# Optimization experiments

Hardware: AMD Instinct MI355X
Metric: run time of the kernel (lower is better)

The kernel has to match this reference:

```python
import jax, jax.numpy as jnp
import numpy as np

LARGENUMBER = 10000.0
B, L = 32, 128


def setup_inputs() -> dict:
    key = jax.random.key(0)
    k1, k2 = jax.random.split(key)
    scores = jax.random.normal(k1, (B, L, L, 1), dtype=jnp.float32)
    seq_lens = jax.random.randint(k2, (B,), L // 2, L + 1).astype(jnp.int32)
    seq_lens = seq_lens.at[0].set(L)  # module assumes max(seq_lens) == matrix dim
    return {"span_mention_score_matrix": scores, "sequence_lengths": seq_lens}


def _inside_logZ(scores, seq_lens):
    """CKY inside algorithm in the log semiring (the `coolio` path).

    Recurrence (combined mention/non-mention channels):
      A[i,i]  = log(1 + e^{s_ii})
      A[i,j]  = logsumexp_{k=i..j-1}(A[i,k] + A[k+1,j]) + log(1 + e^{s_ij})
      Z[b]    = A[b, 0, len_b - 1]
    """
    s = scores[..., 0]                      # (B, L, L)
    Bn, Ln = s.shape[0], s.shape[1]
    log1p_exp = jnp.log1p(jnp.exp(s))       # log(1 + e^s), multiplicative factor per span
    # init: logsumexp([score, 0 above/on diag | -LARGE below diag]) as in coolio
    tri = jnp.where(jnp.arange(Ln)[:, None] <= jnp.arange(Ln)[None, :], 0.0, -LARGENUMBER)
    A0 = jnp.logaddexp(s, tri[None])        # diagonal entries = log(1+e^s); upper entries get overwritten

    i_idx = jnp.arange(Ln)[:, None]         # (L, 1)   span start
    m_idx = jnp.arange(Ln - 1)[None, :]     # (1, L-1) split offset
    rows = jnp.arange(Ln)

    def body(A, w):
        # left child  A[i, i+m], right child A[i+m+1, i+w], m = 0..w-1
        jl = jnp.clip(i_idx + m_idx, 0, Ln - 1)
        ir = jnp.clip(i_idx + m_idx + 1, 0, Ln - 1)
        jr = jnp.clip(i_idx + w, 0, Ln - 1)
        left = A[:, i_idx, jl]              # (B, L, L-1)
        right = A[:, ir, jr]                # (B, L, L-1)
        mask = (m_idx < w) & (i_idx + w < Ln)
        vals = jnp.where(mask, left + right, -LARGENUMBER)
        S = jax.nn.logsumexp(vals, axis=2)  # (B, L) logbmm along diagonal w
        cols = jnp.clip(rows + w, 0, N := Ln - 1) if False else jnp.clip(rows + w, 0, Ln - 1)
        new = S + log1p_exp[:, rows, cols]
        valid = (rows + w) < Ln
        A = A.at[:, rows, cols].set(jnp.where(valid[None, :], new, A[:, rows, cols]))
        return A, None

    A, _ = jax.lax.scan(body, A0, jnp.arange(1, Ln))
    Z = A[jnp.arange(Bn), 0, seq_lens - 1]  # (B,)
    return Z


def reference(span_mention_score_matrix, sequence_lengths):
    # forward returns (log-partition Z, marginals = dZ.sum()/dscores), like coolio()
    Z, vjp_fn = jax.vjp(lambda sc: _inside_logZ(sc, sequence_lengths), span_mention_score_matrix)
    marginal = vjp_fn(jnp.ones_like(Z))[0][..., 0]  # (B, L, L)
    return Z, marginal
```

## Files before the change

### kernel.cpp

```cpp
#include <hip/hip_runtime.h>

#define LL  128
#define STR 131
#define NT  1024

__device__ __forceinline__ float softplus_f(float x) { return log1pf(__expf(x)); }

__device__ __forceinline__ void lds_barrier() {
    asm volatile("s_waitcnt lgkmcnt(0)" ::: "memory");
    __builtin_amdgcn_s_barrier();
    asm volatile("" ::: "memory");
}

extern "C" __global__ __launch_bounds__(NT, 1) void cky_kernel(
    const float* __restrict__ scores,
    const int* __restrict__ seq_lens,
    float* __restrict__ Z_out,
    float* __restrict__ marg_out)
{
    extern __shared__ float smem[];
    float* ALs = smem;
    float* SBs = smem + LL * STR;

    const int b   = blockIdx.x;
    const int tid = threadIdx.x;
    const int i   = tid >> 3;
    const int vl  = tid & 7;
    const float* s = scores + (size_t)b * LL * LL;
    float* marg = marg_out + (size_t)b * LL * LL;
    const int len = seq_lens[b];

    for (int idx = tid; idx < LL * LL; idx += NT) {
        const int r = idx >> 7, c = idx & 127;
        const float sp = softplus_f(s[idx]);
        if (c > r)       SBs[c * STR + r] = sp;
        else if (c == r) ALs[r * STR + r] = sp;
    }
    lds_barrier();

    const float Ai = ALs[i * STR + i];

    float bulk = 0.f, Mreg = Ai;
    if (i + 1 < len) {
        const int j = i + 1;
        const float S = Ai + ALs[j * STR + j];
        const float A = S + SBs[j * STR + i];
        if (vl == 0) {
            ALs[i * STR + j] = A;
            ALs[j * STR + i] = A;
            SBs[i * STR + j] = S;
        }
    }
    lds_barrier();

    for (int w = 2; w < len; ++w) {
        const int j = i + w;
        float a_jm1 = 0.f;
        if (j < len) {
            a_jm1 = ALs[i * STR + (j - 1)];
            const float a_ip1j = ALs[j * STR + (i + 1)];
            const float a_jj   = ALs[j * STR + j];
            const float spv    = SBs[j * STR + i];
            const float acc = bulk
                            + __expf(Ai    + a_ip1j - Mreg)
                            + __expf(a_jm1 + a_jj   - Mreg);
            const float S = Mreg + __logf(acc);
            const float A = S + spv;
            if (vl == 0) {
                ALs[i * STR + j] = A;
                ALs[j * STR + i] = A;
                SBs[i * STR + j] = S;
            }
        }
        float nb = 0.f;
        if (j + 1 < len) {
            const float M = a_jm1;
            const float* Arow = ALs + i * STR;
            const float* Amir = ALs + (j + 1) * STR;
            for (int k = i + 1 + vl; k <= j - 1; k += 8)
                nb += __expf(Arow[k] + Amir[k + 1] - M);
        }
        nb += __shfl_xor(nb, 1); nb += __shfl_xor(nb, 2); nb += __shfl_xor(nb, 4);
        bulk = nb; Mreg = a_jm1;
        lds_barrier();
    }

    if (tid == 0) Z_out[b] = ALs[len - 1];

    const float Arm1 = (i >= 1) ? ALs[(i - 1) * STR + (i - 1)] : 0.f;
    float gbulk = 0.f;
    for (int w = len - 2; w >= 0; --w) {
        const int c = i + w;
        if (c < len) {
            const float Aown  = ALs[i * STR + c];
            const float S_own = (w == 0) ? 0.f : SBs[i * STR + c];
            float acc = gbulk;
            if (c + 1 < len) {
                const float slL  = SBs[i * STR + (c + 1)];
                const float a_c1 = ALs[(c + 1) * STR + (c + 1)];
                acc += __expf(Aown + a_c1 - slL);
            }
            if (i >= 1) {
                const float slR = SBs[(i - 1) * STR + c];
                acc += __expf(Arm1 + Aown - slR);
            }
            const float SL = S_own - __logf(acc);
            if (vl == 0) SBs[i * STR + c] = SL;
        }
        float nb = 0.f;
        if (w >= 1) {
            const int c2 = i + w - 1;
            if (c2 < len) {
                const float Ao2 = ALs[i * STR + c2];
                const float* ArowC = ALs + (c2 + 1) * STR;
                const float* SLrow = SBs + i * STR;
                for (int J = c2 + 2 + vl; J < len; J += 8)
                    nb += __expf(Ao2 + ArowC[J] - SLrow[J]);
                if (i >= 2) {
                    const float* Amir = ALs + (i - 1) * STR;
                    for (int I = vl; I <= i - 2; I += 8)
                        nb += __expf(Amir[I] + Ao2 - SBs[I * STR + c2]);
                }
            }
        }
        nb += __shfl_xor(nb, 1); nb += __shfl_xor(nb, 2); nb += __shfl_xor(nb, 4);
        gbulk = nb;
        lds_barrier();
    }

    for (int idx = tid; idx < LL * LL; idx += NT) {
        const int r = idx >> 7, c = idx & 127;
        float m = 0.f;
        if (c >= r && c < len) {
            const float sp = softplus_f(s[idx]);
            const float G  = __expf(ALs[r * STR + c] - sp - SBs[r * STR + c]);
            m = G * (1.f - __expf(-sp));
        }
        marg[idx] = m;
    }
}

extern "C" void kernel_launch(void* const* d_in, const int* in_sizes, int n_in,
                              void* d_out, int out_size, void* d_ws, size_t ws_size,
                              hipStream_t stream) {
    const float* scores  = (const float*)d_in[0];
    const int* seq_lens  = (const int*)d_in[1];
    const int B = in_sizes[1];
    float* out = (float*)d_out;
    float* Z_out = out;
    float* marg  = out + B;

    const size_t lds_bytes = (size_t)2 * LL * STR * sizeof(float);
    hipFuncSetAttribute((const void*)cky_kernel,
                        hipFuncAttributeMaxDynamicSharedMemorySize,
                        (int)lds_bytes);
    cky_kernel<<<B, NT, lds_bytes, stream>>>(scores, seq_lens, Z_out, marg);
}
```

Baseline: 266.6 us.

## Adapt threads-per-cell group size per diagonal in CKY inside/outside passes

Replaces the fixed 8-lanes-per-span-start mapping with a per-diagonal group size chosen from the number of active cells, so short diagonals get up to 64 lanes each for the split reduction. Partial sums are carried across iterations through a small LDS array instead of registers, since the cell-to-thread mapping now changes each step. This targets idle threads and long serial inner loops on the later diagonals, which dominate the sequential wavefront. In exchange it adds per-iteration group-size computation, wider shuffle reductions and an extra LDS round trip for the carried sums.

```diff
diff --git a/kernel.cpp b/kernel.cpp
--- a/kernel.cpp
+++ b/kernel.cpp
@@ -21,11 +21,10 @@
     extern __shared__ float smem[];
     float* ALs = smem;
     float* SBs = smem + LL * STR;
+    float* BK  = smem + 2 * LL * STR;
 
     const int b   = blockIdx.x;
     const int tid = threadIdx.x;
-    const int i   = tid >> 3;
-    const int vl  = tid & 7;
     const float* s = scores + (size_t)b * LL * LL;
     float* marg = marg_out + (size_t)b * LL * LL;
     const int len = seq_lens[b];
@@ -33,98 +32,95 @@
     for (int idx = tid; idx < LL * LL; idx += NT) {
         const int r = idx >> 7, c = idx & 127;
         const float sp = softplus_f(s[idx]);
-        if (c > r)       SBs[c * STR + r] = sp;
-        else if (c == r) ALs[r * STR + r] = sp;
+        if (c > r)        SBs[c * STR + r] = sp;
+        else if (c == r) { ALs[r * STR + r] = sp; SBs[r * STR + r] = 0.f; }
     }
+    if (tid < LL) BK[tid] = 0.f;
     lds_barrier();
 
-    const float Ai = ALs[i * STR + i];
-
-    float bulk = 0.f, Mreg = Ai;
-    if (i + 1 < len) {
-        const int j = i + 1;
-        const float S = Ai + ALs[j * STR + j];
+    if (tid < len - 1) {
+        const int i = tid, j = i + 1;
+        const float S = ALs[i * STR + i] + ALs[j * STR + j];
         const float A = S + SBs[j * STR + i];
-        if (vl == 0) {
-            ALs[i * STR + j] = A;
-            ALs[j * STR + i] = A;
-            SBs[i * STR + j] = S;
-        }
+        ALs[i * STR + j] = A;  ALs[j * STR + i] = A;  SBs[i * STR + j] = S;
     }
     lds_barrier();
 
     for (int w = 2; w < len; ++w) {
-        const int j = i + w;
-        float a_jm1 = 0.f;
-        if (j < len) {
-            a_jm1 = ALs[i * STR + (j - 1)];
-            const float a_ip1j = ALs[j * STR + (i + 1)];
-            const float a_jj   = ALs[j * STR + j];
-            const float spv    = SBs[j * STR + i];
-            const float acc = bulk
-                            + __expf(Ai    + a_ip1j - Mreg)
-                            + __expf(a_jm1 + a_jj   - Mreg);
-            const float S = Mreg + __logf(acc);
-            const float A = S + spv;
-            if (vl == 0) {
-                ALs[i * STR + j] = A;
-                ALs[j * STR + i] = A;
+        const int cells = len - w;
+        const int cl = (cells > 1) ? (32 - __clz(cells - 1)) : 0;
+        int gsh = 10 - cl; if (gsh > 6) gsh = 6;
+        const int g = 1 << gsh, gid = tid >> gsh, v = tid & (g - 1);
+        if (gid < cells) {
+            const int i = gid, j = i + w;
+            const float M    = ALs[i * STR + (j - 2)];
+            const float Ai   = ALs[i * STR + i];
+            const float ajm1 = ALs[i * STR + (j - 1)];
+            const float aip1 = ALs[j * STR + (i + 1)];
+            const float ajj  = ALs[j * STR + j];
+            const float spv  = SBs[j * STR + i];
+            const float acc  = BK[i]
+                             + __expf(Ai   + aip1 - M)
+                             + __expf(ajm1 + ajj  - M);
+            if (v == 0) {
+                const float S = M + __logf(acc);
+                ALs[i * STR + j] = S + spv;
+                ALs[j * STR + i] = S + spv;
                 SBs[i * STR + j] = S;
             }
         }
         float nb = 0.f;
-        if (j + 1 < len) {
-            const float M = a_jm1;
+        const int cb = cells - 1;
+        if (gid < cb) {
+            const int i = gid, j2 = i + w + 1;
+            const float M2 = ALs[i * STR + (j2 - 2)];
             const float* Arow = ALs + i * STR;
-            const float* Amir = ALs + (j + 1) * STR;
-            for (int k = i + 1 + vl; k <= j - 1; k += 8)
-                nb += __expf(Arow[k] + Amir[k + 1] - M);
+            const float* Amir = ALs + j2 * STR;
+            for (int k = i + 1 + v; k <= j2 - 2; k += g)
+                nb += __expf(Arow[k] + Amir[k + 1] - M2);
         }
-        nb += __shfl_xor(nb, 1); nb += __shfl_xor(nb, 2); nb += __shfl_xor(nb, 4);
-        bulk = nb; Mreg = a_jm1;
+        for (int off = g >> 1; off; off >>= 1) nb += __shfl_xor(nb, off);
+        if (gid < cb && v == 0) BK[gid] = nb;
         lds_barrier();
     }
 
     if (tid == 0) Z_out[b] = ALs[len - 1];
+    if (tid < LL) BK[tid] = 0.f;
+    lds_barrier();
 
-    const float Arm1 = (i >= 1) ? ALs[(i - 1) * STR + (i - 1)] : 0.f;
-    float gbulk = 0.f;
     for (int w = len - 2; w >= 0; --w) {
-        const int c = i + w;
-        if (c < len) {
-            const float Aown  = ALs[i * STR + c];
-            const float S_own = (w == 0) ? 0.f : SBs[i * STR + c];
-            float acc = gbulk;
-            if (c + 1 < len) {
-                const float slL  = SBs[i * STR + (c + 1)];
-                const float a_c1 = ALs[(c + 1) * STR + (c + 1)];
-                acc += __expf(Aown + a_c1 - slL);
-            }
-            if (i >= 1) {
-                const float slR = SBs[(i - 1) * STR + c];
-                acc += __expf(Arm1 + Aown - slR);
-            }
-            const float SL = S_own - __logf(acc);
-            if (vl == 0) SBs[i * STR + c] = SL;
+        const int cb2 = len - w + 1;
+        const int cl = (cb2 > 1) ? (32 - __clz(cb2 - 1)) : 0;
+        int gsh = 10 - cl; if (gsh > 6) gsh = 6;
+        const int g = 1 << gsh, gid = tid >> gsh, v = tid & (g - 1);
+        if (gid < len - w) {
+            const int i = gid, c = i + w;
+            const float Aown = ALs[i * STR + c];
+            const float Sown = SBs[i * STR + c];
+            float acc = BK[i];
+            if (c + 1 < len)
+                acc += __expf(Aown + ALs[(c + 1) * STR + (c + 1)]
+                                   - SBs[i * STR + (c + 1)]);
+            if (i >= 1)
+                acc += __expf(ALs[(i - 1) * STR + (i - 1)] + Aown
+                                   - SBs[(i - 1) * STR + c]);
+            if (v == 0)
+                SBs[i * STR + c] = Sown - __logf(acc);
         }
         float nb = 0.f;
-        if (w >= 1) {
-            const int c2 = i + w - 1;
-            if (c2 < len) {
-                const float Ao2 = ALs[i * STR + c2];
-                const float* ArowC = ALs + (c2 + 1) * STR;
-                const float* SLrow = SBs + i * STR;
-                for (int J = c2 + 2 + vl; J < len; J += 8)
-                    nb += __expf(Ao2 + ArowC[J] - SLrow[J]);
-                if (i >= 2) {
-                    const float* Amir = ALs + (i - 1) * STR;
-                    for (int I = vl; I <= i - 2; I += 8)
-                        nb += __expf(Amir[I] + Ao2 - SBs[I * STR + c2]);
-                }
-            }
+        if (w >= 1 && gid < cb2) {
+            const int i2 = gid, c2 = i2 + w - 1;
+            const float Ao2 = ALs[i2 * STR + c2];
+            const float* ArowC = ALs + (c2 + 1) * STR;
+            const float* SLrow = SBs + i2 * STR;
+            for (int J = c2 + 2 + v; J < len; J += g)
+                nb += __expf(Ao2 + ArowC[J] - SLrow[J]);
+            const float* Amir = ALs + (i2 - 1) * STR;
+            for (int I = v; I <= i2 - 2; I += g)
+                nb += __expf(Amir[I] + Ao2 - SBs[I * STR + c2]);
         }
-        nb += __shfl_xor(nb, 1); nb += __shfl_xor(nb, 2); nb += __shfl_xor(nb, 4);
-        gbulk = nb;
+        for (int off = g >> 1; off; off >>= 1) nb += __shfl_xor(nb, off);
+        if (w >= 1 && gid < cb2 && v == 0) BK[gid] = nb;
         lds_barrier();
     }
 
@@ -150,7 +146,7 @@
     float* Z_out = out;
     float* marg  = out + B;
 
-    const size_t lds_bytes = (size_t)2 * LL * STR * sizeof(float);
+    const size_t lds_bytes = (size_t)(2 * LL * STR + LL) * sizeof(float);
     hipFuncSetAttribute((const void*)cky_kernel,
                         hipFuncAttributeMaxDynamicSharedMemorySize,
                         (int)lds_bytes);
```

Result: slower. 331.2 us (+24.2%).
